# Kernel tuning notes

Hardware: AMD Instinct MI355X
Metric: run time of the kernel (lower is better)

The kernel has to match this reference:

```python
import jax, jax.numpy as jnp
import numpy as np

N_NODES = 500000
N_EDGES = 5000000
IN_CH, OUT_CH = 16, 8


def setup_inputs() -> dict:
    key = jax.random.key(0)
    k1, k2, k3, k4, k5 = jax.random.split(key, 5)
    x = jax.random.normal(k1, (N_NODES, IN_CH), dtype=jnp.float32)
    src = jax.random.randint(k2, (N_EDGES,), 0, N_NODES, dtype=jnp.int64)
    dst = jax.random.randint(k3, (N_EDGES,), 0, N_NODES, dtype=jnp.int64)
    edge_index = jnp.stack([src, dst], axis=0)
    # PyG Linear: weight [out, in], Glorot init; GCNConv bias init zeros
    bound = np.sqrt(6.0 / (IN_CH + OUT_CH))
    W = jax.random.uniform(k4, (OUT_CH, IN_CH), dtype=jnp.float32, minval=-bound, maxval=bound)
    b = jnp.zeros((OUT_CH,), dtype=jnp.float32)
    return {"x": x, "edge_index": edge_index, "W": W, "b": b}


def reference(x, edge_index, W, b):
    """GCNConv(16, 8) with defaults: add_self_loops=True, normalize=True, bias.
    out = D^{-1/2} (A + I) D^{-1/2} X W^T + b, scatter by target index."""
    N = x.shape[0]
    loops = jnp.arange(N, dtype=edge_index.dtype)
    src = jnp.concatenate([edge_index[0], loops])  # [E + N]
    dst = jnp.concatenate([edge_index[1], loops])
    # degree of self-loop-augmented graph, accumulated at target nodes
    deg = jax.ops.segment_sum(jnp.ones(src.shape[0], dtype=x.dtype), dst, num_segments=N)
    dinv = jnp.where(deg > 0, jax.lax.rsqrt(deg), jnp.zeros_like(deg))
    norm = dinv[src] * dinv[dst]  # [E + N]
    h = x @ W.T  # [N, OUT_CH]
    msgs = norm[:, None] * h[src]  # gather + scale, [E + N, OUT_CH]
    out = jax.ops.segment_sum(msgs, dst, num_segments=N) + b
    return out
```

## Files before the change

### kernel.cpp

```cpp
#include <hip/hip_runtime.h>
#include <hip/hip_fp16.h>

#define IN_CH 16
#define OUT_CH 8

#define NT 256
#define EPT 24
#define TILE (NT*EPT)
#define NBUK 512
#define BSHIFT 10
#define BNODES 1024
#define BMASK 1023
#define SRCBITS 19
#define SRCMASK 0x7FFFF
#define CAP 11264
#define RPT 44

__global__ void __launch_bounds__(NT) k_bin(const int4* __restrict__ src4,
                                            const int4* __restrict__ dst4, int E,
                                            int* __restrict__ gcur,
                                            unsigned* __restrict__ gbuf) {
    __shared__ int hist[NBUK];
    __shared__ int lofs[NBUK];
    __shared__ int gofs[NBUK];
    __shared__ int wsum[4];
    __shared__ unsigned stage[TILE];
    __shared__ unsigned short posb[TILE];

    int t = threadIdx.x;
    long base = (long)blockIdx.x * TILE;
    int cnt = E - (int)base;
    if (cnt > TILE) cnt = TILE;

    for (int j = t; j < NBUK; j += NT) hist[j] = 0;
    __syncthreads();

    unsigned v[EPT];
    int bk[EPT];
    int rk[EPT];
#pragma unroll
    for (int k = 0; k < EPT / 4; k++) {
        int i4 = t + k * NT;
        if (4 * i4 < cnt) {
            int4 s = src4[base / 4 + i4];
            int4 d = dst4[base / 4 + i4];
            int ss[4] = {s.x, s.y, s.z, s.w};
            int dd[4] = {d.x, d.y, d.z, d.w};
#pragma unroll
            for (int j = 0; j < 4; j++) {
                int q = 4 * k + j;
                bk[q] = dd[j] >> BSHIFT;
                v[q] = ((unsigned)(dd[j] & BMASK) << SRCBITS) | (unsigned)ss[j];
                rk[q] = atomicAdd(&hist[bk[q]], 1);
            }
        } else {
#pragma unroll
            for (int j = 0; j < 4; j++) bk[4 * k + j] = -1;
        }
    }
    __syncthreads();

    int a0 = hist[2 * t], a1 = hist[2 * t + 1];
    int ts = a0 + a1;
    int lane = t & 63, wv = t >> 6;
    int inc = ts;
#pragma unroll
    for (int d = 1; d < 64; d <<= 1) {
        int y = __shfl_up(inc, d);
        if (lane >= d) inc += y;
    }
    if (lane == 63) wsum[wv] = inc;
    __syncthreads();
    int wpre = 0;
#pragma unroll
    for (int w = 0; w < 4; w++) wpre += (w < wv) ? wsum[w] : 0;
    int excl = wpre + inc - ts;

    lofs[2 * t] = excl;
    lofs[2 * t + 1] = excl + a0;
    if (a0 > 0) gofs[2 * t] = atomicAdd(&gcur[2 * t], a0) - excl;
    if (a1 > 0) gofs[2 * t + 1] = atomicAdd(&gcur[2 * t + 1], a1) - (excl + a0);
    __syncthreads();

#pragma unroll
    for (int k = 0; k < EPT; k++) {
        if (bk[k] >= 0) {
            int slot = lofs[bk[k]] + rk[k];
            stage[slot] = v[k];
            posb[slot] = (unsigned short)bk[k];
        }
    }
    __syncthreads();

#pragma unroll
    for (int k = 0; k < EPT; k++) {
        int idx = t + k * NT;
        if (idx < cnt) {
            int b2 = posb[idx];
            gbuf[(size_t)b2 * CAP + idx + gofs[b2]] = stage[idx];
        }
    }
}

__global__ void __launch_bounds__(NT) k_sort(unsigned* __restrict__ gbuf,
                                             const int* __restrict__ gcur,
                                             const float* __restrict__ x,
                                             const float* __restrict__ W,
                                             float* __restrict__ dinv,
                                             int* __restrict__ offs,
                                             int* __restrict__ cnts,
                                             uint4* __restrict__ hp16, int N) {
    __shared__ unsigned sorted[CAP];
    __shared__ int hist[BNODES];
    __shared__ int wsum[4];
    __shared__ float Ws[OUT_CH * IN_CH];

    int b = blockIdx.x, t = threadIdx.x;
    int cnt = gcur[b];
    unsigned* p = gbuf + (size_t)b * CAP;

    if (t < OUT_CH * IN_CH) Ws[t] = W[t];
    for (int j = t; j < BNODES; j += NT) hist[j] = 0;
    __syncthreads();

    unsigned v[RPT];
    int rk[RPT];
#pragma unroll
    for (int k4 = 0; k4 < RPT / 4; k4++) {
        int idx = 4 * t + k4 * 4 * NT;
        uint4 vv = *(const uint4*)(p + idx);
        unsigned vs[4] = {vv.x, vv.y, vv.z, vv.w};
#pragma unroll
        for (int j = 0; j < 4; j++) {
            int k = 4 * k4 + j;
            if (idx + j < cnt) {
                v[k] = vs[j];
                rk[k] = atomicAdd(&hist[v[k] >> SRCBITS], 1);
            }
        }
    }
    __syncthreads();

    int h0 = hist[4 * t], h1 = hist[4 * t + 1], h2 = hist[4 * t + 2], h3 = hist[4 * t + 3];
    int ts = h0 + h1 + h2 + h3;
    int lane = t & 63, wv = t >> 6;
    int inc = ts;
#pragma unroll
    for (int d = 1; d < 64; d <<= 1) {
        int y = __shfl_up(inc, d);
        if (lane >= d) inc += y;
    }
    if (lane == 63) wsum[wv] = inc;
    __syncthreads();
    int wpre = 0;
#pragma unroll
    for (int w = 0; w < 4; w++) wpre += (w < wv) ? wsum[w] : 0;
    int e0 = wpre + inc - ts;
    int e1 = e0 + h0, e2 = e1 + h1, e3 = e2 + h2;
    hist[4 * t] = e0; hist[4 * t + 1] = e1; hist[4 * t + 2] = e2; hist[4 * t + 3] = e3;

    int nb = b << BSHIFT;
    int n0 = nb + 4 * t;
    int gofs2 = b * CAP;
    float di0 = rsqrtf(1.0f + (float)h0), di1 = rsqrtf(1.0f + (float)h1);
    float di2 = rsqrtf(1.0f + (float)h2), di3 = rsqrtf(1.0f + (float)h3);
    if (n0 + 3 < N) {
        *(int4*)(offs + n0) = make_int4(gofs2 + e0, gofs2 + e1, gofs2 + e2, gofs2 + e3);
        *(int4*)(cnts + n0) = make_int4(h0, h1, h2, h3);
        *(float4*)(dinv + n0) = make_float4(di0, di1, di2, di3);
    } else {
#pragma unroll
        for (int k = 0; k < 4; k++) {
            int n = n0 + k;
            if (n < N) {
                int hv = (k == 0) ? h0 : (k == 1) ? h1 : (k == 2) ? h2 : h3;
                int ev = (k == 0) ? e0 : (k == 1) ? e1 : (k == 2) ? e2 : e3;
                float dv = (k == 0) ? di0 : (k == 1) ? di1 : (k == 2) ? di2 : di3;
                offs[n] = gofs2 + ev;
                cnts[n] = hv;
                dinv[n] = dv;
            }
        }
    }
    __syncthreads();

#pragma unroll
    for (int k = 0; k < RPT; k++) {
        int idx = t + (k % 4) + (k / 4) * 4 * NT;
        (void)idx;
    }
#pragma unroll
    for (int k4 = 0; k4 < RPT / 4; k4++) {
#pragma unroll
        for (int j = 0; j < 4; j++) {
            int k = 4 * k4 + j;
            int idx = 4 * t + k4 * 4 * NT + j;
            if (idx < cnt) {
                int slot = hist[v[k] >> SRCBITS] + rk[k];
                sorted[slot] = v[k] & SRCMASK;
            }
        }
    }
    __syncthreads();

    int full = cnt & ~3;
    for (int i = 4 * t; i < full; i += 4 * NT) {
        uint4 sv = *(const uint4*)&sorted[i];
        *(uint4*)(p + i) = sv;
    }
    for (int i = full + t; i < cnt; i += NT) p[i] = sorted[i];

    float dis[4] = {di0, di1, di2, di3};
#pragma unroll
    for (int k = 0; k < 4; k++) {
        int n = n0 + k;
        if (n >= N) break;
        const float4* xp = (const float4*)(x + (size_t)n * IN_CH);
        float4 a0 = xp[0], a1 = xp[1], a2 = xp[2], a3 = xp[3];
        float xi[IN_CH] = {a0.x, a0.y, a0.z, a0.w, a1.x, a1.y, a1.z, a1.w,
                           a2.x, a2.y, a2.z, a2.w, a3.x, a3.y, a3.z, a3.w};
        float di = dis[k];
        float h[OUT_CH];
#pragma unroll
        for (int o = 0; o < OUT_CH; o++) {
            float s = 0.0f;
#pragma unroll
            for (int i = 0; i < IN_CH; i++) s += xi[i] * Ws[o * IN_CH + i];
            h[o] = s * di;
        }
        union { uint4 u; __half2 h2[4]; } pk;
        pk.h2[0] = __float22half2_rn(make_float2(h[0], h[1]));
        pk.h2[1] = __float22half2_rn(make_float2(h[2], h[3]));
        pk.h2[2] = __float22half2_rn(make_float2(h[4], h[5]));
        pk.h2[3] = __float22half2_rn(make_float2(h[6], h[7]));
        hp16[n] = pk.u;
    }
}

__device__ __forceinline__ void acc_add(float* a, uint4 g) {
    union { uint4 u; __half2 h2[4]; } pk;
    pk.u = g;
    float2 f0 = __half22float2(pk.h2[0]);
    float2 f1 = __half22float2(pk.h2[1]);
    float2 f2 = __half22float2(pk.h2[2]);
    float2 f3 = __half22float2(pk.h2[3]);
    a[0] += f0.x; a[1] += f0.y; a[2] += f1.x; a[3] += f1.y;
    a[4] += f2.x; a[5] += f2.y; a[6] += f3.x; a[7] += f3.y;
}

__global__ void __launch_bounds__(NT) k_gather(const unsigned* __restrict__ gbuf,
                                               const int* __restrict__ offs,
                                               const int* __restrict__ cnts,
                                               const uint4* __restrict__ hp16,
                                               const float* __restrict__ dinv,
                                               const float* __restrict__ bias,
                                               float* __restrict__ out, int N) {
    int tid = blockIdx.x * blockDim.x + threadIdx.x;
    int n = tid >> 2;
    if (n >= N) return;
    int q = tid & 3;

    int beg = offs[n];
    int end = beg + cnts[n];

    float a[OUT_CH] = {0, 0, 0, 0, 0, 0, 0, 0};
    if (q == 0) {
        union { uint4 u; __half2 h2[4]; } pk;
        pk.u = hp16[n];
        float2 f0 = __half22float2(pk.h2[0]);
        float2 f1 = __half22float2(pk.h2[1]);
        float2 f2 = __half22float2(pk.h2[2]);
        float2 f3 = __half22float2(pk.h2[3]);
        a[0] = f0.x; a[1] = f0.y; a[2] = f1.x; a[3] = f1.y;
        a[4] = f2.x; a[5] = f2.y; a[6] = f3.x; a[7] = f3.y;
    }

    int e = beg + q;
    for (; e + 4 < end; e += 8) {
        unsigned s0 = gbuf[e], s1 = gbuf[e + 4];
        uint4 g0 = hp16[s0];
        uint4 g1 = hp16[s1];
        acc_add(a, g0);
        acc_add(a, g1);
    }
    if (e < end) {
        uint4 g0 = hp16[gbuf[e]];
        acc_add(a, g0);
    }

#pragma unroll
    for (int c = 0; c < OUT_CH; c++) {
        a[c] += __shfl_xor(a[c], 1);
        a[c] += __shfl_xor(a[c], 2);
    }

    float di = dinv[n];
    float2 o;
    o.x = a[2 * q + 0] * di + bias[2 * q + 0];
    o.y = a[2 * q + 1] * di + bias[2 * q + 1];
    ((float2*)(out + (size_t)n * OUT_CH))[q] = o;
}

extern "C" void kernel_launch(void* const* d_in, const int* in_sizes, int n_in,
                              void* d_out, int out_size, void* d_ws, size_t ws_size,
                              hipStream_t stream) {
    const float* x  = (const float*)d_in[0];
    const int*   ei = (const int*)d_in[1];
    const float* W  = (const float*)d_in[2];
    const float* b  = (const float*)d_in[3];
    float* out = (float*)d_out;

    const int N = in_sizes[0] / IN_CH;
    const int E = in_sizes[1] / 2;
    const int* src = ei;
    const int* dst = ei + E;

    const int nbuckets = (N + BNODES - 1) >> BSHIFT;

    int*      gcur = (int*)d_ws;
    float*    dinv = (float*)(gcur + NBUK);
    uint4*    hp16 = (uint4*)(dinv + N);
    unsigned* gbuf = (unsigned*)(hp16 + N);
    int*      offs = (int*)(gbuf + (size_t)NBUK * CAP);
    int*      cnts = offs + N;

    const int tiles = (E + TILE - 1) / TILE;
    dim3 blkG((4 * (long)N + NT - 1) / NT);

    hipMemsetAsync(gcur, 0, NBUK * sizeof(int), stream);
    k_bin<<<tiles, NT, 0, stream>>>((const int4*)src, (const int4*)dst, E, gcur, gbuf);
    k_sort<<<nbuckets, NT, 0, stream>>>(gbuf, gcur, x, W, dinv, offs, cnts, hp16, N);
    k_gather<<<blkG, NT, 0, stream>>>(gbuf, offs, cnts, hp16, dinv, b, out, N);
}
```

Before: 222.1 us.

## Split half-precision node features into two channel halves for gather

```diff
diff --git a/kernel.cpp b/kernel.cpp
--- a/kernel.cpp
+++ b/kernel.cpp
@@ -16,6 +16,8 @@
 #define CAP 11264
 #define RPT 44
 
+typedef float __attribute__((ext_vector_type(4))) fv4;
+
 __global__ void __launch_bounds__(NT) k_bin(const int4* __restrict__ src4,
                                             const int4* __restrict__ dst4, int E,
                                             int* __restrict__ gcur,
@@ -109,7 +111,8 @@
                                              float* __restrict__ dinv,
                                              int* __restrict__ offs,
                                              int* __restrict__ cnts,
-                                             uint4* __restrict__ hp16, int N) {
+                                             uint2* __restrict__ hpA,
+                                             uint2* __restrict__ hpB, int N) {
     __shared__ unsigned sorted[CAP];
     __shared__ int hist[BNODES];
     __shared__ int wsum[4];
@@ -185,11 +188,6 @@
     __syncthreads();
 
 #pragma unroll
-    for (int k = 0; k < RPT; k++) {
-        int idx = t + (k % 4) + (k / 4) * 4 * NT;
-        (void)idx;
-    }
-#pragma unroll
     for (int k4 = 0; k4 < RPT / 4; k4++) {
 #pragma unroll
         for (int j = 0; j < 4; j++) {
@@ -228,77 +226,77 @@
             for (int i = 0; i < IN_CH; i++) s += xi[i] * Ws[o * IN_CH + i];
             h[o] = s * di;
         }
-        union { uint4 u; __half2 h2[4]; } pk;
-        pk.h2[0] = __float22half2_rn(make_float2(h[0], h[1]));
-        pk.h2[1] = __float22half2_rn(make_float2(h[2], h[3]));
-        pk.h2[2] = __float22half2_rn(make_float2(h[4], h[5]));
-        pk.h2[3] = __float22half2_rn(make_float2(h[6], h[7]));
-        hp16[n] = pk.u;
-    }
-}
-
-__device__ __forceinline__ void acc_add(float* a, uint4 g) {
-    union { uint4 u; __half2 h2[4]; } pk;
+        union { uint2 u; __half2 h2[2]; } pa, pb;
+        pa.h2[0] = __float22half2_rn(make_float2(h[0], h[1]));
+        pa.h2[1] = __float22half2_rn(make_float2(h[2], h[3]));
+        pb.h2[0] = __float22half2_rn(make_float2(h[4], h[5]));
+        pb.h2[1] = __float22half2_rn(make_float2(h[6], h[7]));
+        hpA[n] = pa.u;
+        hpB[n] = pb.u;
+    }
+}
+
+__device__ __forceinline__ void acc_add4(float* a, uint2 g) {
+    union { uint2 u; __half2 h2[2]; } pk;
     pk.u = g;
     float2 f0 = __half22float2(pk.h2[0]);
     float2 f1 = __half22float2(pk.h2[1]);
-    float2 f2 = __half22float2(pk.h2[2]);
-    float2 f3 = __half22float2(pk.h2[3]);
     a[0] += f0.x; a[1] += f0.y; a[2] += f1.x; a[3] += f1.y;
-    a[4] += f2.x; a[5] += f2.y; a[6] += f3.x; a[7] += f3.y;
 }
 
 __global__ void __launch_bounds__(NT) k_gather(const unsigned* __restrict__ gbuf,
                                                const int* __restrict__ offs,
                                                const int* __restrict__ cnts,
-                                               const uint4* __restrict__ hp16,
+                                               const uint2* __restrict__ hpA,
+                                               const uint2* __restrict__ hpB,
                                                const float* __restrict__ dinv,
                                                const float* __restrict__ bias,
                                                float* __restrict__ out, int N) {
-    int tid = blockIdx.x * blockDim.x + threadIdx.x;
-    int n = tid >> 2;
+    int b = blockIdx.x;
+    int half = (b >> 2) & 1;
+    int logical = (b >> 3) * 4 + (b & 3);
+    long ltid = (long)logical * NT + threadIdx.x;
+    int n = (int)(ltid >> 1);
     if (n >= N) return;
-    int q = tid & 3;
+    int q = (int)ltid & 1;
+
+    const uint2* __restrict__ hp = half ? hpB : hpA;
 
     int beg = offs[n];
     int end = beg + cnts[n];
 
-    float a[OUT_CH] = {0, 0, 0, 0, 0, 0, 0, 0};
+    float a[4] = {0, 0, 0, 0};
+    if (q == 0) acc_add4(a, hp[n]);
+
+    int e = beg + q;
+    for (; e + 6 < end; e += 8) {
+        unsigned s0 = __builtin_nontemporal_load(gbuf + e);
+        unsigned s1 = __builtin_nontemporal_load(gbuf + e + 2);
+        unsigned s2 = __builtin_nontemporal_load(gbuf + e + 4);
+        unsigned s3 = __builtin_nontemporal_load(gbuf + e + 6);
+        uint2 g0 = hp[s0];
+        uint2 g1 = hp[s1];
+        uint2 g2 = hp[s2];
+        uint2 g3 = hp[s3];
+        acc_add4(a, g0); acc_add4(a, g1); acc_add4(a, g2); acc_add4(a, g3);
+    }
+    for (; e < end; e += 2) {
+        uint2 g0 = hp[__builtin_nontemporal_load(gbuf + e)];
+        acc_add4(a, g0);
+    }
+
+#pragma unroll
+    for (int c = 0; c < 4; c++) a[c] += __shfl_xor(a[c], 1);
+
     if (q == 0) {
-        union { uint4 u; __half2 h2[4]; } pk;
-        pk.u = hp16[n];
-        float2 f0 = __half22float2(pk.h2[0]);
-        float2 f1 = __half22float2(pk.h2[1]);
-        float2 f2 = __half22float2(pk.h2[2]);
-        float2 f3 = __half22float2(pk.h2[3]);
-        a[0] = f0.x; a[1] = f0.y; a[2] = f1.x; a[3] = f1.y;
-        a[4] = f2.x; a[5] = f2.y; a[6] = f3.x; a[7] = f3.y;
-    }
-
-    int e = beg + q;
-    for (; e + 4 < end; e += 8) {
-        unsigned s0 = gbuf[e], s1 = gbuf[e + 4];
-        uint4 g0 = hp16[s0];
-        uint4 g1 = hp16[s1];
-        acc_add(a, g0);
-        acc_add(a, g1);
-    }
-    if (e < end) {
-        uint4 g0 = hp16[gbuf[e]];
-        acc_add(a, g0);
-    }
-
-#pragma unroll
-    for (int c = 0; c < OUT_CH; c++) {
-        a[c] += __shfl_xor(a[c], 1);
-        a[c] += __shfl_xor(a[c], 2);
-    }
-
-    float di = dinv[n];
-    float2 o;
-    o.x = a[2 * q + 0] * di + bias[2 * q + 0];
-    o.y = a[2 * q + 1] * di + bias[2 * q + 1];
-    ((float2*)(out + (size_t)n * OUT_CH))[q] = o;
+        float di = dinv[n];
+        fv4 o;
+        o[0] = a[0] * di + bias[4 * half + 0];
+        o[1] = a[1] * di + bias[4 * half + 1];
+        o[2] = a[2] * di + bias[4 * half + 2];
+        o[3] = a[3] * di + bias[4 * half + 3];
+        __builtin_nontemporal_store(o, (fv4*)(out + (size_t)n * OUT_CH + 4 * half));
+    }
 }
 
 extern "C" void kernel_launch(void* const* d_in, const int* in_sizes, int n_in,
@@ -319,16 +317,19 @@
 
     int*      gcur = (int*)d_ws;
     float*    dinv = (float*)(gcur + NBUK);
-    uint4*    hp16 = (uint4*)(dinv + N);
-    unsigned* gbuf = (unsigned*)(hp16 + N);
+    uint2*    hpA  = (uint2*)(dinv + N);
+    uint2*    hpB  = hpA + N;
+    unsigned* gbuf = (unsigned*)(hpB + N);
     int*      offs = (int*)(gbuf + (size_t)NBUK * CAP);
     int*      cnts = offs + N;
 
     const int tiles = (E + TILE - 1) / TILE;
-    dim3 blkG((4 * (long)N + NT - 1) / NT);
-
-    hipMemsetAsync(gcur, 0, NBUK * sizeof(int), stream);
+
+    const int bph = (2 * N + NT - 1) / NT;
+    int gblocks = ((2 * bph + 7) / 8) * 8;
+
+    (void)hipMemsetAsync(gcur, 0, NBUK * sizeof(int), stream);
     k_bin<<<tiles, NT, 0, stream>>>((const int4*)src, (const int4*)dst, E, gcur, gbuf);
-    k_sort<<<nbuckets, NT, 0, stream>>>(gbuf, gcur, x, W, dinv, offs, cnts, hp16, N);
-    k_gather<<<blkG, NT, 0, stream>>>(gbuf, offs, cnts, hp16, dinv, b, out, N);
-}
+    k_sort<<<nbuckets, NT, 0, stream>>>(gbuf, gcur, x, W, dinv, offs, cnts, hpA, hpB, N);
+    k_gather<<<gblocks, NT, 0, stream>>>(gbuf, offs, cnts, hpA, hpB, dinv, b, out, N);
+}
```

After: 256.7 us. 15.6% more time.

## Fuse bucket sort with neighbor gather, splitting degree and transform into own kernel

Applied to the files above, without the earlier changes.

```diff
diff --git a/kernel.cpp b/kernel.cpp
--- a/kernel.cpp
+++ b/kernel.cpp
@@ -16,6 +16,8 @@
 #define CAP 11264
 #define RPT 44
 
+typedef float __attribute__((ext_vector_type(4))) fv4;
+
 __global__ void __launch_bounds__(NT) k_bin(const int4* __restrict__ src4,
                                             const int4* __restrict__ dst4, int E,
                                             int* __restrict__ gcur,
@@ -102,124 +104,42 @@
     }
 }
 
-__global__ void __launch_bounds__(NT) k_sort(unsigned* __restrict__ gbuf,
-                                             const int* __restrict__ gcur,
-                                             const float* __restrict__ x,
-                                             const float* __restrict__ W,
-                                             float* __restrict__ dinv,
-                                             int* __restrict__ offs,
-                                             int* __restrict__ cnts,
-                                             uint4* __restrict__ hp16, int N) {
-    __shared__ unsigned sorted[CAP];
+__global__ void __launch_bounds__(NT) k_degtrans(const unsigned* __restrict__ gbuf,
+                                                 const int* __restrict__ gcur,
+                                                 const float* __restrict__ x,
+                                                 const float* __restrict__ W,
+                                                 uint4* __restrict__ hp16, int N) {
     __shared__ int hist[BNODES];
-    __shared__ int wsum[4];
     __shared__ float Ws[OUT_CH * IN_CH];
 
     int b = blockIdx.x, t = threadIdx.x;
     int cnt = gcur[b];
-    unsigned* p = gbuf + (size_t)b * CAP;
+    const unsigned* p = gbuf + (size_t)b * CAP;
 
     if (t < OUT_CH * IN_CH) Ws[t] = W[t];
     for (int j = t; j < BNODES; j += NT) hist[j] = 0;
     __syncthreads();
 
-    unsigned v[RPT];
-    int rk[RPT];
-#pragma unroll
-    for (int k4 = 0; k4 < RPT / 4; k4++) {
-        int idx = 4 * t + k4 * 4 * NT;
-        uint4 vv = *(const uint4*)(p + idx);
+    int n4 = (cnt + 3) >> 2;
+    for (int i4 = t; i4 < n4; i4 += NT) {
+        uint4 vv = *(const uint4*)(p + 4 * i4);
         unsigned vs[4] = {vv.x, vv.y, vv.z, vv.w};
 #pragma unroll
-        for (int j = 0; j < 4; j++) {
-            int k = 4 * k4 + j;
-            if (idx + j < cnt) {
-                v[k] = vs[j];
-                rk[k] = atomicAdd(&hist[v[k] >> SRCBITS], 1);
-            }
-        }
-    }
-    __syncthreads();
-
-    int h0 = hist[4 * t], h1 = hist[4 * t + 1], h2 = hist[4 * t + 2], h3 = hist[4 * t + 3];
-    int ts = h0 + h1 + h2 + h3;
-    int lane = t & 63, wv = t >> 6;
-    int inc = ts;
-#pragma unroll
-    for (int d = 1; d < 64; d <<= 1) {
-        int y = __shfl_up(inc, d);
-        if (lane >= d) inc += y;
-    }
-    if (lane == 63) wsum[wv] = inc;
-    __syncthreads();
-    int wpre = 0;
-#pragma unroll
-    for (int w = 0; w < 4; w++) wpre += (w < wv) ? wsum[w] : 0;
-    int e0 = wpre + inc - ts;
-    int e1 = e0 + h0, e2 = e1 + h1, e3 = e2 + h2;
-    hist[4 * t] = e0; hist[4 * t + 1] = e1; hist[4 * t + 2] = e2; hist[4 * t + 3] = e3;
-
-    int nb = b << BSHIFT;
-    int n0 = nb + 4 * t;
-    int gofs2 = b * CAP;
-    float di0 = rsqrtf(1.0f + (float)h0), di1 = rsqrtf(1.0f + (float)h1);
-    float di2 = rsqrtf(1.0f + (float)h2), di3 = rsqrtf(1.0f + (float)h3);
-    if (n0 + 3 < N) {
-        *(int4*)(offs + n0) = make_int4(gofs2 + e0, gofs2 + e1, gofs2 + e2, gofs2 + e3);
-        *(int4*)(cnts + n0) = make_int4(h0, h1, h2, h3);
-        *(float4*)(dinv + n0) = make_float4(di0, di1, di2, di3);
-    } else {
-#pragma unroll
-        for (int k = 0; k < 4; k++) {
-            int n = n0 + k;
-            if (n < N) {
-                int hv = (k == 0) ? h0 : (k == 1) ? h1 : (k == 2) ? h2 : h3;
-                int ev = (k == 0) ? e0 : (k == 1) ? e1 : (k == 2) ? e2 : e3;
-                float dv = (k == 0) ? di0 : (k == 1) ? di1 : (k == 2) ? di2 : di3;
-                offs[n] = gofs2 + ev;
-                cnts[n] = hv;
-                dinv[n] = dv;
-            }
-        }
-    }
-    __syncthreads();
-
-#pragma unroll
-    for (int k = 0; k < RPT; k++) {
-        int idx = t + (k % 4) + (k / 4) * 4 * NT;
-        (void)idx;
-    }
-#pragma unroll
-    for (int k4 = 0; k4 < RPT / 4; k4++) {
-#pragma unroll
-        for (int j = 0; j < 4; j++) {
-            int k = 4 * k4 + j;
-            int idx = 4 * t + k4 * 4 * NT + j;
-            if (idx < cnt) {
-                int slot = hist[v[k] >> SRCBITS] + rk[k];
-                sorted[slot] = v[k] & SRCMASK;
-            }
-        }
-    }
-    __syncthreads();
-
-    int full = cnt & ~3;
-    for (int i = 4 * t; i < full; i += 4 * NT) {
-        uint4 sv = *(const uint4*)&sorted[i];
-        *(uint4*)(p + i) = sv;
-    }
-    for (int i = full + t; i < cnt; i += NT) p[i] = sorted[i];
-
-    float dis[4] = {di0, di1, di2, di3};
+        for (int j = 0; j < 4; j++)
+            if (4 * i4 + j < cnt) atomicAdd(&hist[vs[j] >> SRCBITS], 1);
+    }
+    __syncthreads();
+
+    int n0 = (b << BSHIFT) + 4 * t;
 #pragma unroll
     for (int k = 0; k < 4; k++) {
         int n = n0 + k;
         if (n >= N) break;
+        float di = rsqrtf(1.0f + (float)hist[4 * t + k]);
         const float4* xp = (const float4*)(x + (size_t)n * IN_CH);
         float4 a0 = xp[0], a1 = xp[1], a2 = xp[2], a3 = xp[3];
         float xi[IN_CH] = {a0.x, a0.y, a0.z, a0.w, a1.x, a1.y, a1.z, a1.w,
                            a2.x, a2.y, a2.z, a2.w, a3.x, a3.y, a3.z, a3.w};
-        float di = dis[k];
         float h[OUT_CH];
 #pragma unroll
         for (int o = 0; o < OUT_CH; o++) {
@@ -248,57 +168,126 @@
     a[4] += f2.x; a[5] += f2.y; a[6] += f3.x; a[7] += f3.y;
 }
 
-__global__ void __launch_bounds__(NT) k_gather(const unsigned* __restrict__ gbuf,
-                                               const int* __restrict__ offs,
-                                               const int* __restrict__ cnts,
-                                               const uint4* __restrict__ hp16,
-                                               const float* __restrict__ dinv,
-                                               const float* __restrict__ bias,
-                                               float* __restrict__ out, int N) {
-    int tid = blockIdx.x * blockDim.x + threadIdx.x;
-    int n = tid >> 2;
-    if (n >= N) return;
-    int q = tid & 3;
-
-    int beg = offs[n];
-    int end = beg + cnts[n];
-
-    float a[OUT_CH] = {0, 0, 0, 0, 0, 0, 0, 0};
-    if (q == 0) {
-        union { uint4 u; __half2 h2[4]; } pk;
-        pk.u = hp16[n];
-        float2 f0 = __half22float2(pk.h2[0]);
-        float2 f1 = __half22float2(pk.h2[1]);
-        float2 f2 = __half22float2(pk.h2[2]);
-        float2 f3 = __half22float2(pk.h2[3]);
-        a[0] = f0.x; a[1] = f0.y; a[2] = f1.x; a[3] = f1.y;
-        a[4] = f2.x; a[5] = f2.y; a[6] = f3.x; a[7] = f3.y;
-    }
-
-    int e = beg + q;
-    for (; e + 4 < end; e += 8) {
-        unsigned s0 = gbuf[e], s1 = gbuf[e + 4];
-        uint4 g0 = hp16[s0];
-        uint4 g1 = hp16[s1];
-        acc_add(a, g0);
-        acc_add(a, g1);
-    }
-    if (e < end) {
-        uint4 g0 = hp16[gbuf[e]];
-        acc_add(a, g0);
-    }
-
-#pragma unroll
-    for (int c = 0; c < OUT_CH; c++) {
-        a[c] += __shfl_xor(a[c], 1);
-        a[c] += __shfl_xor(a[c], 2);
-    }
-
-    float di = dinv[n];
-    float2 o;
-    o.x = a[2 * q + 0] * di + bias[2 * q + 0];
-    o.y = a[2 * q + 1] * di + bias[2 * q + 1];
-    ((float2*)(out + (size_t)n * OUT_CH))[q] = o;
+__global__ void __launch_bounds__(NT) k_sortgather(const unsigned* __restrict__ gbuf,
+                                                   const int* __restrict__ gcur,
+                                                   const uint4* __restrict__ hp16,
+                                                   const float* __restrict__ bias,
+                                                   float* __restrict__ out, int N) {
+    __shared__ unsigned sorted[CAP];
+    __shared__ int hist[BNODES];
+    __shared__ int wsum[4];
+
+    int b = blockIdx.x, t = threadIdx.x;
+    int cnt = gcur[b];
+    const unsigned* p = gbuf + (size_t)b * CAP;
+
+    for (int j = t; j < BNODES; j += NT) hist[j] = 0;
+    __syncthreads();
+
+    unsigned v[RPT];
+    int rk[RPT];
+#pragma unroll
+    for (int k4 = 0; k4 < RPT / 4; k4++) {
+        int idx = 4 * t + k4 * 4 * NT;
+        uint4 vv = *(const uint4*)(p + idx);
+        unsigned vs[4] = {vv.x, vv.y, vv.z, vv.w};
+#pragma unroll
+        for (int j = 0; j < 4; j++) {
+            int k = 4 * k4 + j;
+            if (idx + j < cnt) {
+                v[k] = vs[j];
+                rk[k] = atomicAdd(&hist[v[k] >> SRCBITS], 1);
+            }
+        }
+    }
+    __syncthreads();
+
+    int h0 = hist[4 * t], h1 = hist[4 * t + 1], h2 = hist[4 * t + 2], h3 = hist[4 * t + 3];
+    int ts = h0 + h1 + h2 + h3;
+    int lane = t & 63, wv = t >> 6;
+    int inc = ts;
+#pragma unroll
+    for (int d = 1; d < 64; d <<= 1) {
+        int y = __shfl_up(inc, d);
+        if (lane >= d) inc += y;
+    }
+    if (lane == 63) wsum[wv] = inc;
+    __syncthreads();
+    int wpre = 0;
+#pragma unroll
+    for (int w = 0; w < 4; w++) wpre += (w < wv) ? wsum[w] : 0;
+    int e0 = wpre + inc - ts;
+    int e1 = e0 + h0, e2 = e1 + h1, e3 = e2 + h2;
+    hist[4 * t] = e0; hist[4 * t + 1] = e1; hist[4 * t + 2] = e2; hist[4 * t + 3] = e3;
+    __syncthreads();
+
+#pragma unroll
+    for (int k4 = 0; k4 < RPT / 4; k4++) {
+#pragma unroll
+        for (int j = 0; j < 4; j++) {
+            int k = 4 * k4 + j;
+            int idx = 4 * t + k4 * 4 * NT + j;
+            if (idx < cnt) {
+                int slot = hist[v[k] >> SRCBITS] + rk[k];
+                sorted[slot] = v[k] & SRCMASK;
+            }
+        }
+    }
+    __syncthreads();
+
+    int n0 = (b << BSHIFT) + 4 * t;
+    int eS[4] = {e0, e1, e2, e3};
+    int hS[4] = {h0, h1, h2, h3};
+
+    float bb[OUT_CH];
+#pragma unroll
+    for (int o = 0; o < OUT_CH; o++) bb[o] = bias[o];
+
+#pragma unroll
+    for (int k = 0; k < 4; k++) {
+        int n = n0 + k;
+        if (n >= N) break;
+
+        float a[OUT_CH];
+        acc_add((float*)a, hp16[n]);
+#pragma unroll
+        for (int o = 0; o < OUT_CH; o++) a[o] = a[o];
+        {
+            union { uint4 u; __half2 h2[4]; } pk;
+            pk.u = hp16[n];
+            float2 f0 = __half22float2(pk.h2[0]);
+            float2 f1 = __half22float2(pk.h2[1]);
+            float2 f2 = __half22float2(pk.h2[2]);
+            float2 f3 = __half22float2(pk.h2[3]);
+            a[0] = f0.x; a[1] = f0.y; a[2] = f1.x; a[3] = f1.y;
+            a[4] = f2.x; a[5] = f2.y; a[6] = f3.x; a[7] = f3.y;
+        }
+
+        int e = eS[k], end = eS[k] + hS[k];
+        for (; e + 3 < end; e += 4) {
+            unsigned s0 = sorted[e], s1 = sorted[e + 1];
+            unsigned s2 = sorted[e + 2], s3 = sorted[e + 3];
+            uint4 g0 = hp16[s0];
+            uint4 g1 = hp16[s1];
+            uint4 g2 = hp16[s2];
+            uint4 g3 = hp16[s3];
+            acc_add(a, g0); acc_add(a, g1); acc_add(a, g2); acc_add(a, g3);
+        }
+        for (; e < end; e++) {
+            uint4 g0 = hp16[sorted[e]];
+            acc_add(a, g0);
+        }
+
+        float di = rsqrtf(1.0f + (float)hS[k]);
+        fv4 o0, o1;
+#pragma unroll
+        for (int j = 0; j < 4; j++) {
+            o0[j] = a[j] * di + bb[j];
+            o1[j] = a[4 + j] * di + bb[4 + j];
+        }
+        __builtin_nontemporal_store(o0, (fv4*)(out + (size_t)n * OUT_CH));
+        __builtin_nontemporal_store(o1, (fv4*)(out + (size_t)n * OUT_CH) + 1);
+    }
 }
 
 extern "C" void kernel_launch(void* const* d_in, const int* in_sizes, int n_in,
@@ -318,17 +307,13 @@
     const int nbuckets = (N + BNODES - 1) >> BSHIFT;
 
     int*      gcur = (int*)d_ws;
-    float*    dinv = (float*)(gcur + NBUK);
-    uint4*    hp16 = (uint4*)(dinv + N);
+    uint4*    hp16 = (uint4*)(gcur + NBUK);
     unsigned* gbuf = (unsigned*)(hp16 + N);
-    int*      offs = (int*)(gbuf + (size_t)NBUK * CAP);
-    int*      cnts = offs + N;
 
     const int tiles = (E + TILE - 1) / TILE;
-    dim3 blkG((4 * (long)N + NT - 1) / NT);
-
-    hipMemsetAsync(gcur, 0, NBUK * sizeof(int), stream);
+
+    (void)hipMemsetAsync(gcur, 0, NBUK * sizeof(int), stream);
     k_bin<<<tiles, NT, 0, stream>>>((const int4*)src, (const int4*)dst, E, gcur, gbuf);
-    k_sort<<<nbuckets, NT, 0, stream>>>(gbuf, gcur, x, W, dinv, offs, cnts, hp16, N);
-    k_gather<<<blkG, NT, 0, stream>>>(gbuf, offs, cnts, hp16, dinv, b, out, N);
-}
+    k_degtrans<<<nbuckets, NT, 0, stream>>>(gbuf, gcur, x, W, hp16, N);
+    k_sortgather<<<nbuckets, NT, 0, stream>>>(gbuf, gcur, hp16, b, out, N);
+}
```

New measurement: 215.1 us. 1.03x faster.
